# Performance work log

Measured on AMD Instinct MI355X. Metric: run time of the kernel, lower is better.

Reference implementation:

```python
import jax, jax.numpy as jnp
import numpy as np

N = 4096          # reservoir_size
D = 64            # base_input_dim (feedback=0 so input_dim == base_input_dim)
O = 64            # output_dim
T = 4096          # sequence length
SPECTRAL_RADIUS = 0.9
SPARSITY = 0.1
INPUT_SCALING = 1.0
BIAS_SCALING = 0.2
LEAK = 0.8        # leak_rate


def setup_inputs() -> dict:
    key = jax.random.key(0)
    k0, k1, k2, k3, k4, k5 = jax.random.split(key, 6)
    # Sparse recurrent matrix scaled so spectral radius ~= SPECTRAL_RADIUS
    # (circular law: radius ~ std * sqrt(N * density))
    std = SPECTRAL_RADIUS / np.sqrt(N * SPARSITY)
    W = jax.random.normal(k0, (N, N), dtype=jnp.float32) * std
    mask = jax.random.bernoulli(k1, SPARSITY, (N, N))
    W = W * mask.astype(jnp.float32)
    W_in = jax.random.uniform(k2, (N, D), dtype=jnp.float32,
                              minval=-INPUT_SCALING, maxval=INPUT_SCALING)
    b = jax.random.uniform(k3, (N,), dtype=jnp.float32,
                           minval=-BIAS_SCALING, maxval=BIAS_SCALING)
    # Trained readout (here: random stand-in), acts on [x, 1]
    W_out = jax.random.normal(k4, (O, N + 1), dtype=jnp.float32) * 0.02
    inputs = jax.random.normal(k5, (T, D), dtype=jnp.float32)
    return {"inputs": inputs, "W": W, "W_in": W_in, "b": b, "W_out": W_out}


def reference(inputs, W, W_in, b, W_out):
    """ESN.forward with feedback=0, washout=0: leaky-integrator reservoir
    recurrence + affine readout per timestep, as a single lax.scan."""
    Wo = W_out[:, :-1]   # (O, N)
    bo = W_out[:, -1]    # (O,)

    def step(x, u):
        # x: (N,) reservoir state; u: (D,) input at time t
        pre = W @ x + W_in @ u + b
        x_new = (1.0 - LEAK) * x + LEAK * jnp.tanh(pre)
        y = Wo @ x_new + bo   # W_out @ cat([x, 1])
        return x_new, y

    x0 = jnp.zeros((W.shape[0],), dtype=inputs.dtype)
    _, ys = jax.lax.scan(step, x0, inputs)
    return ys  # (T, O)
```

## Files before the change

### kernel.cpp

```cpp
#include <hip/hip_runtime.h>

constexpr int N_ = 4096;
constexpr int D_ = 64;
constexpr int O_ = 64;
constexpr int T_ = 4096;
constexpr float LEAK_ = 0.8f;
constexpr int NBLK = 256;
constexpr int NTHR = 1024;
constexpr int NWAVE = 16;
constexpr int RPB = N_ / NBLK;
constexpr int KELL = 512;
constexpr int GRP = KELL / 64;
constexpr int PDEPTH = 8;
constexpr int SPT = N_ / NTHR;

typedef unsigned long long u64;
#define LD64(p)   __hip_atomic_load((const u64*)(p), __ATOMIC_RELAXED, __HIP_MEMORY_SCOPE_AGENT)
#define ST64(p,v) __hip_atomic_store((u64*)(p), (v), __ATOMIC_RELAXED, __HIP_MEMORY_SCOPE_AGENT)

__device__ __forceinline__ u64 mkpair(float x, unsigned seq) {
    return ((u64)seq << 32) | (u64)__float_as_uint(x);
}
__device__ __forceinline__ unsigned pseq(u64 v) { return (unsigned)(v >> 32); }
__device__ __forceinline__ float pval(u64 v) { return __uint_as_float((unsigned)v); }

__global__ void esn_prep(const float* __restrict__ W_out,
                         float* __restrict__ WoT, float* __restrict__ bo) {
    int idx = blockIdx.x * blockDim.x + threadIdx.x;
    if (idx < N_ * O_) {
        int row = idx / O_;
        int o = idx - row * O_;
        WoT[idx] = W_out[o * (N_ + 1) + row];
    }
    if (idx < O_) bo[idx] = W_out[idx * (N_ + 1) + N_];
}

__global__ __launch_bounds__(64) void esn_sparsify(
    const float* __restrict__ W,
    unsigned short* __restrict__ cols, float* __restrict__ vals) {
    const int row = blockIdx.x;
    const int lane = threadIdx.x;
    __shared__ unsigned short nnz_c[KELL];
    __shared__ float nnz_w[KELL];
    __shared__ short slot_nnz[KELL];
    for (int s = lane; s < KELL; s += 64) slot_nnz[s] = -1;

    const float* Wr = W + (size_t)row * N_;
    const unsigned long long ltmask = (1ull << lane) - 1ull;
    int cnt = 0;
    for (int c0 = 0; c0 < N_; c0 += 64) {
        float w = Wr[c0 + lane];
        unsigned long long m = __ballot(w != 0.0f);
        if (w != 0.0f) {
            int pos = cnt + __popcll(m & ltmask);
            if (pos < KELL) { nnz_c[pos] = (unsigned short)(c0 + lane); nnz_w[pos] = w; }
        }
        cnt += __popcll(m);
    }
    if (cnt > KELL) cnt = KELL;
    __syncthreads();

    if (lane == 0) {
        unsigned char fill[GRP];
        unsigned char nxt[32];
        for (int g = 0; g < GRP; ++g) fill[g] = 0;
        for (int bnk = 0; bnk < 32; ++bnk) nxt[bnk] = 0;
        for (int i = 0; i < cnt; ++i) {
            int bnk = nnz_c[i] & 31;
            int g = nxt[bnk];
            int tries = 0;
            while (fill[g] >= 64 && tries < GRP) { g = (g + 1) % GRP; ++tries; }
            slot_nnz[g * 64 + fill[g]] = (short)i;
            fill[g]++;
            nxt[bnk] = (unsigned char)((g + 1) % GRP);
        }
    }
    __syncthreads();

    unsigned short* crow = cols + (size_t)row * KELL;
    float* vrow = vals + (size_t)row * KELL;
    for (int s = lane; s < KELL; s += 64) {
        int i = slot_nnz[s];
        crow[s] = (i >= 0) ? nnz_c[i] : 0;
        vrow[s] = (i >= 0) ? nnz_w[i] : 0.0f;
    }
}

__global__ __launch_bounds__(NTHR) void esn_main(
    const float* __restrict__ inputs,
    const unsigned short* __restrict__ cols, const float* __restrict__ vals,
    const float* __restrict__ W_in, const float* __restrict__ b,
    const float* __restrict__ WoT, const float* __restrict__ bo,
    float* __restrict__ y, u64* __restrict__ xpairs, u64* __restrict__ ppairs)
{
    __shared__ float x_lds[2][N_];
    __shared__ float u_lds[2][D_];
    __shared__ float pw_lds[2][NWAVE][O_];
    const int tid = threadIdx.x;
    const int bid = blockIdx.x;
    const int wave = tid >> 6;
    const int lane = tid & 63;
    const int row = bid * RPB + wave;

    unsigned short cc[GRP];
    float vv[GRP];
    #pragma unroll
    for (int j = 0; j < GRP; ++j) {
        cc[j] = cols[(size_t)row * KELL + 64 * j + lane];
        vv[j] = vals[(size_t)row * KELL + 64 * j + lane];
    }
    const float win  = W_in[row * D_ + lane];
    const float brow = b[row];
    const float wo   = WoT[row * O_ + lane];

    #pragma unroll
    for (int k = 0; k < SPT; ++k) x_lds[0][tid + k * NTHR] = 0.f;
    if (tid < D_) u_lds[0][tid] = inputs[tid];
    __syncthreads();

    float xo = 0.f;

    for (int t = 0; t < T_; ++t) {
        const int pt = t & 1;

        float acc = 0.f;
        #pragma unroll
        for (int j = 0; j < GRP; ++j) acc += vv[j] * x_lds[pt][cc[j]];
        acc += win * u_lds[pt][lane];
        #pragma unroll
        for (int off = 32; off; off >>= 1) acc += __shfl_xor(acc, off);
        float xn = (1.f - LEAK_) * xo + LEAK_ * tanhf(acc + brow);
        xo = xn;

        if (lane == 0)
            ST64(&xpairs[(size_t)pt * N_ + row], mkpair(xn, (unsigned)(t + 1)));

        pw_lds[pt][wave][lane] = wo * xn;
        if (t + 1 < T_ && tid < D_) u_lds[pt ^ 1][tid] = inputs[(t + 1) * D_ + tid];

        {
            const u64* xp = xpairs + (size_t)pt * N_;
            const unsigned tgt = (unsigned)(t + 1);
            u64 v[SPT];
            #pragma unroll
            for (int k = 0; k < SPT; ++k) v[k] = LD64(&xp[tid + k * NTHR]);
            while (true) {
                int stale = 0;
                #pragma unroll
                for (int k = 0; k < SPT; ++k)
                    if (pseq(v[k]) != tgt) { v[k] = LD64(&xp[tid + k * NTHR]); stale = 1; }
                if (__ballot(stale) == 0ull) break;
            }
            #pragma unroll
            for (int k = 0; k < SPT; ++k)
                x_lds[pt ^ 1][tid + k * NTHR] = pval(v[k]);
        }
        __syncthreads();

        if (wave == 1) {
            float s = 0.f;
            #pragma unroll
            for (int w = 0; w < NWAVE; ++w) s += pw_lds[pt][w][lane];
            ST64(&ppairs[(size_t)(t & (PDEPTH - 1)) * (NBLK * O_) + bid * O_ + lane],
                 mkpair(s, (unsigned)(t + 1)));
        } else if (wave == 2 && t >= 2 && bid < O_) {
            const u64* pp = ppairs + (size_t)((t - 2) & (PDEPTH - 1)) * (NBLK * O_);
            const unsigned tgt = (unsigned)(t - 1);
            u64 v0 = LD64(&pp[lane * O_ + bid]);
            u64 v1 = LD64(&pp[(lane + 64) * O_ + bid]);
            u64 v2 = LD64(&pp[(lane + 128) * O_ + bid]);
            u64 v3 = LD64(&pp[(lane + 192) * O_ + bid]);
            while (true) {
                int stale = 0;
                if (pseq(v0) != tgt) { v0 = LD64(&pp[lane * O_ + bid]); stale = 1; }
                if (pseq(v1) != tgt) { v1 = LD64(&pp[(lane + 64) * O_ + bid]); stale = 1; }
                if (pseq(v2) != tgt) { v2 = LD64(&pp[(lane + 128) * O_ + bid]); stale = 1; }
                if (pseq(v3) != tgt) { v3 = LD64(&pp[(lane + 192) * O_ + bid]); stale = 1; }
                if (__ballot(stale) == 0ull) break;
            }
            float s = pval(v0) + pval(v1) + pval(v2) + pval(v3);
            #pragma unroll
            for (int off = 32; off; off >>= 1) s += __shfl_xor(s, off);
            if (lane == 0) y[(t - 2) * O_ + bid] = s + bo[bid];
        }
    }

    if (wave == 2 && bid < O_) {
        for (int tt = T_ - 2; tt < T_; ++tt) {
            const u64* pp = ppairs + (size_t)(tt & (PDEPTH - 1)) * (NBLK * O_);
            const unsigned tgt = (unsigned)(tt + 1);
            u64 v0 = LD64(&pp[lane * O_ + bid]);
            u64 v1 = LD64(&pp[(lane + 64) * O_ + bid]);
            u64 v2 = LD64(&pp[(lane + 128) * O_ + bid]);
            u64 v3 = LD64(&pp[(lane + 192) * O_ + bid]);
            while (true) {
                int stale = 0;
                if (pseq(v0) != tgt) { v0 = LD64(&pp[lane * O_ + bid]); stale = 1; }
                if (pseq(v1) != tgt) { v1 = LD64(&pp[(lane + 64) * O_ + bid]); stale = 1; }
                if (pseq(v2) != tgt) { v2 = LD64(&pp[(lane + 128) * O_ + bid]); stale = 1; }
                if (pseq(v3) != tgt) { v3 = LD64(&pp[(lane + 192) * O_ + bid]); stale = 1; }
                if (__ballot(stale) == 0ull) break;
            }
            float s = pval(v0) + pval(v1) + pval(v2) + pval(v3);
            #pragma unroll
            for (int off = 32; off; off >>= 1) s += __shfl_xor(s, off);
            if (lane == 0) y[tt * O_ + bid] = s + bo[bid];
        }
    }
}

extern "C" void kernel_launch(void* const* d_in, const int* in_sizes, int n_in,
                              void* d_out, int out_size, void* d_ws, size_t ws_size,
                              hipStream_t stream) {
    const float* inputs = (const float*)d_in[0];
    const float* W      = (const float*)d_in[1];
    const float* W_in   = (const float*)d_in[2];
    const float* b      = (const float*)d_in[3];
    const float* W_out  = (const float*)d_in[4];
    float* y  = (float*)d_out;

    u64* xpairs = (u64*)d_ws;
    u64* ppairs = xpairs + 2 * N_;
    float* WoT  = (float*)(ppairs + (size_t)PDEPTH * NBLK * O_);
    float* bo   = WoT + N_ * O_;
    float* vals = bo + O_;
    unsigned short* cols = (unsigned short*)(vals + (size_t)N_ * KELL);

    size_t seq_bytes = (2 * N_ + (size_t)PDEPTH * NBLK * O_) * sizeof(u64);
    hipMemsetAsync(d_ws, 0, seq_bytes, stream);

    hipLaunchKernelGGL(esn_prep, dim3((N_ * O_ + 255) / 256), dim3(256),
                       0, stream, W_out, WoT, bo);
    hipLaunchKernelGGL(esn_sparsify, dim3(N_), dim3(64),
                       0, stream, W, cols, vals);

    hipLaunchKernelGGL(esn_main, dim3(NBLK), dim3(NTHR), 0, stream,
                       inputs, cols, vals, W_in, b, WoT, bo, y,
                       xpairs, ppairs);
}
```

Before: 13.66 ms.

## Specialize waves: split x gather, readout reduction and input load before single barrier

Restricts the spin-wait gather of the new reservoir state to 8 waves, and gives the per-block readout partial sum, the cross-block output reduction and the next-input load to dedicated idle waves (8, 9, 10). These now run in the same phase as the gather, one step later, so each step has a single barrier and less serial work after it. Each gathering wave now handles twice as many state entries. The readout pipeline gets an extra step of lag, and the epilogue drains three pending steps.

```diff
diff --git a/kernel.cpp b/kernel.cpp
--- a/kernel.cpp
+++ b/kernel.cpp
@@ -12,7 +12,8 @@
 constexpr int KELL = 512;
 constexpr int GRP = KELL / 64;
 constexpr int PDEPTH = 8;
-constexpr int SPT = N_ / NTHR;
+constexpr int PWAVES = 8;
+constexpr int XSPT = N_ / (PWAVES * 64);
 
 typedef unsigned long long u64;
 #define LD64(p)   __hip_atomic_load((const u64*)(p), __ATOMIC_RELAXED, __HIP_MEMORY_SCOPE_AGENT)
@@ -114,7 +115,7 @@
     const float wo   = WoT[row * O_ + lane];
 
     #pragma unroll
-    for (int k = 0; k < SPT; ++k) x_lds[0][tid + k * NTHR] = 0.f;
+    for (int k = 0; k < 4; ++k) x_lds[0][tid + k * NTHR] = 0.f;
     if (tid < D_) u_lds[0][tid] = inputs[tid];
     __syncthreads();
 
@@ -134,59 +135,69 @@
 
         if (lane == 0)
             ST64(&xpairs[(size_t)pt * N_ + row], mkpair(xn, (unsigned)(t + 1)));
-
         pw_lds[pt][wave][lane] = wo * xn;
-        if (t + 1 < T_ && tid < D_) u_lds[pt ^ 1][tid] = inputs[(t + 1) * D_ + tid];
-
-        {
+
+        if (wave < PWAVES) {
             const u64* xp = xpairs + (size_t)pt * N_;
             const unsigned tgt = (unsigned)(t + 1);
-            u64 v[SPT];
+            u64 v[XSPT];
             #pragma unroll
-            for (int k = 0; k < SPT; ++k) v[k] = LD64(&xp[tid + k * NTHR]);
+            for (int k = 0; k < XSPT; ++k) v[k] = LD64(&xp[tid + k * 512]);
             while (true) {
                 int stale = 0;
                 #pragma unroll
-                for (int k = 0; k < SPT; ++k)
-                    if (pseq(v[k]) != tgt) { v[k] = LD64(&xp[tid + k * NTHR]); stale = 1; }
+                for (int k = 0; k < XSPT; ++k)
+                    if (pseq(v[k]) != tgt) { v[k] = LD64(&xp[tid + k * 512]); stale = 1; }
                 if (__ballot(stale) == 0ull) break;
             }
             #pragma unroll
-            for (int k = 0; k < SPT; ++k)
-                x_lds[pt ^ 1][tid + k * NTHR] = pval(v[k]);
+            for (int k = 0; k < XSPT; ++k)
+                x_lds[pt ^ 1][tid + k * 512] = pval(v[k]);
+        } else if (wave == 8) {
+            if (t >= 1) {
+                float s = 0.f;
+                #pragma unroll
+                for (int w = 0; w < NWAVE; ++w) s += pw_lds[pt ^ 1][w][lane];
+                ST64(&ppairs[(size_t)((t - 1) & (PDEPTH - 1)) * (NBLK * O_) + bid * O_ + lane],
+                     mkpair(s, (unsigned)t));
+            }
+        } else if (wave == 9) {
+            if (t >= 3 && bid < O_) {
+                const int tt = t - 3;
+                const u64* pp = ppairs + (size_t)(tt & (PDEPTH - 1)) * (NBLK * O_);
+                const unsigned tgt = (unsigned)(tt + 1);
+                u64 v0 = LD64(&pp[lane * O_ + bid]);
+                u64 v1 = LD64(&pp[(lane + 64) * O_ + bid]);
+                u64 v2 = LD64(&pp[(lane + 128) * O_ + bid]);
+                u64 v3 = LD64(&pp[(lane + 192) * O_ + bid]);
+                while (true) {
+                    int stale = 0;
+                    if (pseq(v0) != tgt) { v0 = LD64(&pp[lane * O_ + bid]); stale = 1; }
+                    if (pseq(v1) != tgt) { v1 = LD64(&pp[(lane + 64) * O_ + bid]); stale = 1; }
+                    if (pseq(v2) != tgt) { v2 = LD64(&pp[(lane + 128) * O_ + bid]); stale = 1; }
+                    if (pseq(v3) != tgt) { v3 = LD64(&pp[(lane + 192) * O_ + bid]); stale = 1; }
+                    if (__ballot(stale) == 0ull) break;
+                }
+                float s = pval(v0) + pval(v1) + pval(v2) + pval(v3);
+                #pragma unroll
+                for (int off = 32; off; off >>= 1) s += __shfl_xor(s, off);
+                if (lane == 0) y[tt * O_ + bid] = s + bo[bid];
+            }
+        } else if (wave == 10) {
+            if (t + 1 < T_ && lane < D_) u_lds[pt ^ 1][lane] = inputs[(t + 1) * D_ + lane];
         }
         __syncthreads();
-
-        if (wave == 1) {
-            float s = 0.f;
-            #pragma unroll
-            for (int w = 0; w < NWAVE; ++w) s += pw_lds[pt][w][lane];
-            ST64(&ppairs[(size_t)(t & (PDEPTH - 1)) * (NBLK * O_) + bid * O_ + lane],
-                 mkpair(s, (unsigned)(t + 1)));
-        } else if (wave == 2 && t >= 2 && bid < O_) {
-            const u64* pp = ppairs + (size_t)((t - 2) & (PDEPTH - 1)) * (NBLK * O_);
-            const unsigned tgt = (unsigned)(t - 1);
-            u64 v0 = LD64(&pp[lane * O_ + bid]);
-            u64 v1 = LD64(&pp[(lane + 64) * O_ + bid]);
-            u64 v2 = LD64(&pp[(lane + 128) * O_ + bid]);
-            u64 v3 = LD64(&pp[(lane + 192) * O_ + bid]);
-            while (true) {
-                int stale = 0;
-                if (pseq(v0) != tgt) { v0 = LD64(&pp[lane * O_ + bid]); stale = 1; }
-                if (pseq(v1) != tgt) { v1 = LD64(&pp[(lane + 64) * O_ + bid]); stale = 1; }
-                if (pseq(v2) != tgt) { v2 = LD64(&pp[(lane + 128) * O_ + bid]); stale = 1; }
-                if (pseq(v3) != tgt) { v3 = LD64(&pp[(lane + 192) * O_ + bid]); stale = 1; }
-                if (__ballot(stale) == 0ull) break;
-            }
-            float s = pval(v0) + pval(v1) + pval(v2) + pval(v3);
-            #pragma unroll
-            for (int off = 32; off; off >>= 1) s += __shfl_xor(s, off);
-            if (lane == 0) y[(t - 2) * O_ + bid] = s + bo[bid];
-        }
-    }
-
-    if (wave == 2 && bid < O_) {
-        for (int tt = T_ - 2; tt < T_; ++tt) {
+    }
+
+    if (wave == 8) {
+        float s = 0.f;
+        #pragma unroll
+        for (int w = 0; w < NWAVE; ++w) s += pw_lds[(T_ - 1) & 1][w][lane];
+        ST64(&ppairs[(size_t)((T_ - 1) & (PDEPTH - 1)) * (NBLK * O_) + bid * O_ + lane],
+             mkpair(s, (unsigned)T_));
+    }
+    if (wave == 9 && bid < O_) {
+        for (int tt = T_ - 3; tt < T_; ++tt) {
             const u64* pp = ppairs + (size_t)(tt & (PDEPTH - 1)) * (NBLK * O_);
             const unsigned tgt = (unsigned)(tt + 1);
             u64 v0 = LD64(&pp[lane * O_ + bid]);
```

Result: slower. 20.52 ms (+50.2%).

## Halve block count by assigning two reservoir rows per wave

Applied to the files above, without the earlier changes.

The persistent kernel now runs 128 blocks instead of 256, with each wave computing two reservoir rows (two sparse dot products, interleaved shuffle reductions, paired tanh updates). This halves the number of blocks that publish and poll the global state each step, and the readout reducer reads only 128 partial sums per output. The cost is more work and more registers per wave on each step's critical path, and fewer CUs in use.

```diff
diff --git a/kernel.cpp b/kernel.cpp
--- a/kernel.cpp
+++ b/kernel.cpp
@@ -5,14 +5,15 @@
 constexpr int O_ = 64;
 constexpr int T_ = 4096;
 constexpr float LEAK_ = 0.8f;
-constexpr int NBLK = 256;
+constexpr int NBLK = 128;
 constexpr int NTHR = 1024;
 constexpr int NWAVE = 16;
 constexpr int RPB = N_ / NBLK;
+constexpr int RPW = 2;
 constexpr int KELL = 512;
 constexpr int GRP = KELL / 64;
 constexpr int PDEPTH = 8;
-constexpr int SPT = N_ / NTHR;
+constexpr int XSPT = N_ / NTHR;
 
 typedef unsigned long long u64;
 #define LD64(p)   __hip_atomic_load((const u64*)(p), __ATOMIC_RELAXED, __HIP_MEMORY_SCOPE_AGENT)
@@ -100,59 +101,73 @@
     const int bid = blockIdx.x;
     const int wave = tid >> 6;
     const int lane = tid & 63;
-    const int row = bid * RPB + wave;
-
-    unsigned short cc[GRP];
-    float vv[GRP];
+    const int row0 = bid * RPB + wave * RPW;
+
+    unsigned short cc0[GRP], cc1[GRP];
+    float vv0[GRP], vv1[GRP];
     #pragma unroll
     for (int j = 0; j < GRP; ++j) {
-        cc[j] = cols[(size_t)row * KELL + 64 * j + lane];
-        vv[j] = vals[(size_t)row * KELL + 64 * j + lane];
-    }
-    const float win  = W_in[row * D_ + lane];
-    const float brow = b[row];
-    const float wo   = WoT[row * O_ + lane];
+        cc0[j] = cols[(size_t)row0 * KELL + 64 * j + lane];
+        vv0[j] = vals[(size_t)row0 * KELL + 64 * j + lane];
+        cc1[j] = cols[(size_t)(row0 + 1) * KELL + 64 * j + lane];
+        vv1[j] = vals[(size_t)(row0 + 1) * KELL + 64 * j + lane];
+    }
+    const float win0 = W_in[row0 * D_ + lane];
+    const float win1 = W_in[(row0 + 1) * D_ + lane];
+    const float br0  = b[row0];
+    const float br1  = b[row0 + 1];
+    const float wo0  = WoT[row0 * O_ + lane];
+    const float wo1  = WoT[(row0 + 1) * O_ + lane];
 
     #pragma unroll
-    for (int k = 0; k < SPT; ++k) x_lds[0][tid + k * NTHR] = 0.f;
+    for (int k = 0; k < 4; ++k) x_lds[0][tid + k * NTHR] = 0.f;
     if (tid < D_) u_lds[0][tid] = inputs[tid];
     __syncthreads();
 
-    float xo = 0.f;
+    float xo0 = 0.f, xo1 = 0.f;
 
     for (int t = 0; t < T_; ++t) {
         const int pt = t & 1;
 
-        float acc = 0.f;
+        float acc0 = 0.f, acc1 = 0.f;
         #pragma unroll
-        for (int j = 0; j < GRP; ++j) acc += vv[j] * x_lds[pt][cc[j]];
-        acc += win * u_lds[pt][lane];
+        for (int j = 0; j < GRP; ++j) acc0 += vv0[j] * x_lds[pt][cc0[j]];
         #pragma unroll
-        for (int off = 32; off; off >>= 1) acc += __shfl_xor(acc, off);
-        float xn = (1.f - LEAK_) * xo + LEAK_ * tanhf(acc + brow);
-        xo = xn;
-
-        if (lane == 0)
-            ST64(&xpairs[(size_t)pt * N_ + row], mkpair(xn, (unsigned)(t + 1)));
-
-        pw_lds[pt][wave][lane] = wo * xn;
+        for (int j = 0; j < GRP; ++j) acc1 += vv1[j] * x_lds[pt][cc1[j]];
+        const float uv = u_lds[pt][lane];
+        acc0 += win0 * uv;
+        acc1 += win1 * uv;
+        #pragma unroll
+        for (int off = 32; off; off >>= 1) {
+            acc0 += __shfl_xor(acc0, off);
+            acc1 += __shfl_xor(acc1, off);
+        }
+        float xn0 = (1.f - LEAK_) * xo0 + LEAK_ * tanhf(acc0 + br0);
+        float xn1 = (1.f - LEAK_) * xo1 + LEAK_ * tanhf(acc1 + br1);
+        xo0 = xn0; xo1 = xn1;
+
+        if (lane < RPW)
+            ST64(&xpairs[(size_t)pt * N_ + row0 + lane],
+                 mkpair(lane ? xn1 : xn0, (unsigned)(t + 1)));
+        pw_lds[pt][wave][lane] = wo0 * xn0 + wo1 * xn1;
+
         if (t + 1 < T_ && tid < D_) u_lds[pt ^ 1][tid] = inputs[(t + 1) * D_ + tid];
 
         {
             const u64* xp = xpairs + (size_t)pt * N_;
             const unsigned tgt = (unsigned)(t + 1);
-            u64 v[SPT];
-            #pragma unroll
-            for (int k = 0; k < SPT; ++k) v[k] = LD64(&xp[tid + k * NTHR]);
+            u64 v[XSPT];
+            #pragma unroll
+            for (int k = 0; k < XSPT; ++k) v[k] = LD64(&xp[tid + k * NTHR]);
             while (true) {
                 int stale = 0;
                 #pragma unroll
-                for (int k = 0; k < SPT; ++k)
+                for (int k = 0; k < XSPT; ++k)
                     if (pseq(v[k]) != tgt) { v[k] = LD64(&xp[tid + k * NTHR]); stale = 1; }
                 if (__ballot(stale) == 0ull) break;
             }
             #pragma unroll
-            for (int k = 0; k < SPT; ++k)
+            for (int k = 0; k < XSPT; ++k)
                 x_lds[pt ^ 1][tid + k * NTHR] = pval(v[k]);
         }
         __syncthreads();
@@ -168,17 +183,13 @@
             const unsigned tgt = (unsigned)(t - 1);
             u64 v0 = LD64(&pp[lane * O_ + bid]);
             u64 v1 = LD64(&pp[(lane + 64) * O_ + bid]);
-            u64 v2 = LD64(&pp[(lane + 128) * O_ + bid]);
-            u64 v3 = LD64(&pp[(lane + 192) * O_ + bid]);
             while (true) {
                 int stale = 0;
                 if (pseq(v0) != tgt) { v0 = LD64(&pp[lane * O_ + bid]); stale = 1; }
                 if (pseq(v1) != tgt) { v1 = LD64(&pp[(lane + 64) * O_ + bid]); stale = 1; }
-                if (pseq(v2) != tgt) { v2 = LD64(&pp[(lane + 128) * O_ + bid]); stale = 1; }
-                if (pseq(v3) != tgt) { v3 = LD64(&pp[(lane + 192) * O_ + bid]); stale = 1; }
                 if (__ballot(stale) == 0ull) break;
             }
-            float s = pval(v0) + pval(v1) + pval(v2) + pval(v3);
+            float s = pval(v0) + pval(v1);
             #pragma unroll
             for (int off = 32; off; off >>= 1) s += __shfl_xor(s, off);
             if (lane == 0) y[(t - 2) * O_ + bid] = s + bo[bid];
@@ -191,17 +202,13 @@
             const unsigned tgt = (unsigned)(tt + 1);
             u64 v0 = LD64(&pp[lane * O_ + bid]);
             u64 v1 = LD64(&pp[(lane + 64) * O_ + bid]);
-            u64 v2 = LD64(&pp[(lane + 128) * O_ + bid]);
-            u64 v3 = LD64(&pp[(lane + 192) * O_ + bid]);
             while (true) {
                 int stale = 0;
                 if (pseq(v0) != tgt) { v0 = LD64(&pp[lane * O_ + bid]); stale = 1; }
                 if (pseq(v1) != tgt) { v1 = LD64(&pp[(lane + 64) * O_ + bid]); stale = 1; }
-                if (pseq(v2) != tgt) { v2 = LD64(&pp[(lane + 128) * O_ + bid]); stale = 1; }
-                if (pseq(v3) != tgt) { v3 = LD64(&pp[(lane + 192) * O_ + bid]); stale = 1; }
                 if (__ballot(stale) == 0ull) break;
             }
-            float s = pval(v0) + pval(v1) + pval(v2) + pval(v3);
+            float s = pval(v0) + pval(v1);
             #pragma unroll
             for (int off = 32; off; off >>= 1) s += __shfl_xor(s, off);
             if (lane == 0) y[tt * O_ + bid] = s + bo[bid];
```

Measured after the change: 17.10 ms. 25.2% more time.

## Add per-block sent counters to gate polling of recurrent state exchange

Applied to the files above, without the earlier changes.

Adds a per-block 'sent' sequence counter that each block publishes after a block-wide barrier. Each wave first polls the 16 counters covering the state rows it will read, then loads those 256 rows with sequence checks. Before, every thread spun directly on its 4 state pairs. The goal is to cut global polling traffic on the state pairs by spinning on fewer, compact counters. The cost is an extra __syncthreads and a second global handshake per timestep on the critical path.

```diff
diff --git a/kernel.cpp b/kernel.cpp
--- a/kernel.cpp
+++ b/kernel.cpp
@@ -12,11 +12,13 @@
 constexpr int KELL = 512;
 constexpr int GRP = KELL / 64;
 constexpr int PDEPTH = 8;
-constexpr int SPT = N_ / NTHR;
+constexpr int BPW = NBLK / NWAVE;
 
 typedef unsigned long long u64;
 #define LD64(p)   __hip_atomic_load((const u64*)(p), __ATOMIC_RELAXED, __HIP_MEMORY_SCOPE_AGENT)
 #define ST64(p,v) __hip_atomic_store((u64*)(p), (v), __ATOMIC_RELAXED, __HIP_MEMORY_SCOPE_AGENT)
+#define LD32(p)   __hip_atomic_load((const unsigned*)(p), __ATOMIC_RELAXED, __HIP_MEMORY_SCOPE_AGENT)
+#define ST32(p,v) __hip_atomic_store((unsigned*)(p), (v), __ATOMIC_RELAXED, __HIP_MEMORY_SCOPE_AGENT)
 
 __device__ __forceinline__ u64 mkpair(float x, unsigned seq) {
     return ((u64)seq << 32) | (u64)__float_as_uint(x);
@@ -91,7 +93,8 @@
     const unsigned short* __restrict__ cols, const float* __restrict__ vals,
     const float* __restrict__ W_in, const float* __restrict__ b,
     const float* __restrict__ WoT, const float* __restrict__ bo,
-    float* __restrict__ y, u64* __restrict__ xpairs, u64* __restrict__ ppairs)
+    float* __restrict__ y, u64* __restrict__ xpairs, u64* __restrict__ ppairs,
+    unsigned* __restrict__ sent)
 {
     __shared__ float x_lds[2][N_];
     __shared__ float u_lds[2][D_];
@@ -114,7 +117,7 @@
     const float wo   = WoT[row * O_ + lane];
 
     #pragma unroll
-    for (int k = 0; k < SPT; ++k) x_lds[0][tid + k * NTHR] = 0.f;
+    for (int k = 0; k < 4; ++k) x_lds[0][tid + k * NTHR] = 0.f;
     if (tid < D_) u_lds[0][tid] = inputs[tid];
     __syncthreads();
 
@@ -134,27 +137,39 @@
 
         if (lane == 0)
             ST64(&xpairs[(size_t)pt * N_ + row], mkpair(xn, (unsigned)(t + 1)));
-
         pw_lds[pt][wave][lane] = wo * xn;
-        if (t + 1 < T_ && tid < D_) u_lds[pt ^ 1][tid] = inputs[(t + 1) * D_ + tid];
+
+        float uv_pf = 0.f;
+        if (wave == 3 && t + 1 < T_) uv_pf = inputs[(t + 1) * D_ + lane];
+
+        __syncthreads();
+
+        if (tid == 0) ST32(&sent[bid], (unsigned)(t + 1));
 
         {
-            const u64* xp = xpairs + (size_t)pt * N_;
             const unsigned tgt = (unsigned)(t + 1);
-            u64 v[SPT];
-            #pragma unroll
-            for (int k = 0; k < SPT; ++k) v[k] = LD64(&xp[tid + k * NTHR]);
+            while (__ballot(lane < BPW &&
+                            LD32(&sent[wave * BPW + lane]) < tgt) != 0ull) {}
+        }
+
+        {
+            const u64* xp = xpairs + (size_t)pt * N_ + wave * (BPW * RPB);
+            const unsigned tgt = (unsigned)(t + 1);
+            u64 v[4];
+            #pragma unroll
+            for (int k = 0; k < 4; ++k) v[k] = LD64(&xp[k * 64 + lane]);
             while (true) {
                 int stale = 0;
                 #pragma unroll
-                for (int k = 0; k < SPT; ++k)
-                    if (pseq(v[k]) != tgt) { v[k] = LD64(&xp[tid + k * NTHR]); stale = 1; }
+                for (int k = 0; k < 4; ++k)
+                    if (pseq(v[k]) != tgt) { v[k] = LD64(&xp[k * 64 + lane]); stale = 1; }
                 if (__ballot(stale) == 0ull) break;
             }
             #pragma unroll
-            for (int k = 0; k < SPT; ++k)
-                x_lds[pt ^ 1][tid + k * NTHR] = pval(v[k]);
-        }
+            for (int k = 0; k < 4; ++k)
+                x_lds[pt ^ 1][wave * (BPW * RPB) + k * 64 + lane] = pval(v[k]);
+        }
+        if (wave == 3 && t + 1 < T_) u_lds[pt ^ 1][lane] = uv_pf;
         __syncthreads();
 
         if (wave == 1) {
@@ -221,12 +236,13 @@
 
     u64* xpairs = (u64*)d_ws;
     u64* ppairs = xpairs + 2 * N_;
-    float* WoT  = (float*)(ppairs + (size_t)PDEPTH * NBLK * O_);
+    unsigned* sent = (unsigned*)(ppairs + (size_t)PDEPTH * NBLK * O_);
+    float* WoT  = (float*)((char*)sent + 4096);
     float* bo   = WoT + N_ * O_;
     float* vals = bo + O_;
     unsigned short* cols = (unsigned short*)(vals + (size_t)N_ * KELL);
 
-    size_t seq_bytes = (2 * N_ + (size_t)PDEPTH * NBLK * O_) * sizeof(u64);
+    size_t seq_bytes = (2 * N_ + (size_t)PDEPTH * NBLK * O_) * sizeof(u64) + 4096;
     hipMemsetAsync(d_ws, 0, seq_bytes, stream);
 
     hipLaunchKernelGGL(esn_prep, dim3((N_ * O_ + 255) / 256), dim3(256),
@@ -236,5 +252,5 @@
 
     hipLaunchKernelGGL(esn_main, dim3(NBLK), dim3(NTHR), 0, stream,
                        inputs, cols, vals, W_in, b, WoT, bo, y,
-                       xpairs, ppairs);
-}
+                       xpairs, ppairs, sent);
+}
```

After: 23.85 ms. 74.6% more time.
